# Kernel tuning notes

Measured on AMD Instinct MI355X. Metric: run time of the kernel, lower is better.

## Reference

```python
import jax, jax.numpy as jnp
import numpy as np

# Circuit geometry (matches QNN(sequence_length=16384, quantum_layer_quantity=4, output_quantity=64, entangler='basic'))
SEQ_LEN = 16384
N_ADDR = 14                      # ceil(log2(16384))
N_DATA = 4                       # UNIQUE_NUCLEOTIDE_QUANTITY
N_WIRES = N_ADDR + N_DATA        # 18
DIM = 2 ** N_WIRES               # 262144
N_LAYERS = 4
OUT = 64
BATCH = 32


def _apply_rx(state, theta, w):
    """Apply RX(theta) on wire w (wire 0 = most significant bit)."""
    c = jnp.cos(theta / 2).astype(jnp.complex64)
    s = (-1j * jnp.sin(theta / 2)).astype(jnp.complex64)
    U = jnp.stack([jnp.stack([c, s]), jnp.stack([s, c])])  # [2,2]
    B = state.shape[0]
    st = state.reshape(B, 2 ** w, 2, -1)
    st = jnp.einsum('ij,bajc->baic', U, st)
    return st.reshape(B, DIM)


def _apply_cnot(state, c, t):
    """CNOT with control wire c, target wire t."""
    B = state.shape[0]
    st = state.reshape((B,) + (2,) * N_WIRES)
    c_ax, t_ax = 1 + c, 1 + t
    p0 = jnp.take(st, 0, axis=c_ax)
    p1 = jnp.take(st, 1, axis=c_ax)
    t_ax_r = t_ax - 1 if t_ax > c_ax else t_ax
    p1 = jnp.flip(p1, axis=t_ax_r)  # X on target within control=1 block
    st = jnp.stack([p0, p1], axis=c_ax)
    return st.reshape(B, DIM)


def _circuit_probs(x, qweights):
    # Encoding: address register stays |0...0>, so among all multi-controlled
    # BasisEmbeddings only index 0 (control pattern all zeros) applies its X
    # gates. Resulting basis state index = bits of x[:,0,:] on the 4 data
    # wires (least-significant bits), address bits = 0.
    bits = x[:, 0, :]  # [B, 4]
    pw = jnp.asarray([8, 4, 2, 1], dtype=jnp.int32)
    idx = jnp.sum(bits * pw, axis=-1)  # [B]
    state = jax.nn.one_hot(idx, DIM, dtype=jnp.complex64)  # [B, DIM]
    # BasicEntanglerLayers: per layer, RX on every wire then a CNOT ring.
    for l in range(N_LAYERS):
        for w in range(N_WIRES):
            state = _apply_rx(state, qweights[l, w], w)
        for w in range(N_WIRES):
            state = _apply_cnot(state, w, (w + 1) % N_WIRES)
    return jnp.abs(state) ** 2  # qml.probs over all wires -> [B, DIM] float32


def setup_inputs() -> dict:
    key = jax.random.key(0)
    kx, kw, kW = jax.random.split(key, 3)
    x = jax.random.randint(kx, (BATCH, SEQ_LEN, N_DATA), 0, 2, dtype=jnp.int32)
    qweights = jax.random.uniform(kw, (N_LAYERS, N_WIRES), dtype=jnp.float32,
                                  maxval=2.0 * np.pi)
    W = jax.random.normal(kW, (OUT, DIM), dtype=jnp.float32) / np.sqrt(DIM)
    b = jnp.zeros((OUT,), dtype=jnp.float32)
    return {"x": x, "qweights": qweights, "W": W, "b": b}


def reference(x, qweights, W, b):
    probs = _circuit_probs(x, qweights)          # [B, 2^18]
    logits = probs @ W.T + b                     # [B, 64]
    return jax.nn.sigmoid(logits)
```

## Files before the change

kernel.cpp:

```cpp
#include <hip/hip_runtime.h>
#include <math.h>


#define DIM (1 << 18)
#define NW 18
#define CH 128
#define CPB 4
#define NMM 512
#define PAD16(i) ((i) + ((i) >> 4))

typedef short short8 __attribute__((ext_vector_type(8)));
typedef float f32x4  __attribute__((ext_vector_type(4)));

__device__ __forceinline__ unsigned perm18(unsigned i) {
    unsigned s = i;
    s ^= s >> 1; s ^= s >> 2; s ^= s >> 4; s ^= s >> 8; s ^= s >> 16;
    unsigned out = s & 0x1FFFFu;
    out |= ((s ^ (i >> 17)) & 1u) << 17;
    return out;
}
__device__ __forceinline__ unsigned pinv18(unsigned b) {
    unsigned t = b & 0x1FFFFu;
    unsigned u = (t ^ (t >> 1)) & 0xFFFFu;
    unsigned i17 = ((b >> 17) ^ t) & 1u;
    unsigned i16 = ((t >> 16) ^ i17) & 1u;
    return u | (i16 << 16) | (i17 << 17);
}
__device__ __forceinline__ void bfly(float2& a0, float2& a1, float c, float s) {
    float2 n0 = make_float2(c * a0.x + s * a1.y, c * a0.y - s * a1.x);
    float2 n1 = make_float2(c * a1.x + s * a0.y, c * a1.y - s * a0.x);
    a0 = n0; a1 = n1;
}
__device__ __forceinline__ short f2bf(float x) {
    unsigned u = __float_as_uint(x);
    return (short)((u + 0x7FFFu + ((u >> 16) & 1u)) >> 16);
}

constexpr unsigned cX1M[33] = {
    0x001,0x002,0x004,0x008,0x010,0x020,0x040,0x080,0x100,0x200,0x400,0x800,
    0xC01,0xC03,0xC06,0xC0C,0xC18,0xC30,0xC60,0xCC0,0xD80,0xA00,0xC00,
    0xA01,0x602,0x605,0x60A,0x614,0x628,0x650,0x6A0,0x740,0x600};
constexpr unsigned char cX1A[33] = {
    35,34,33,32,31,30,29,28,27,20,19,18,
    53,52,51,50,49,48,47,46,45,37,36,
    71,70,69,68,67,66,65,64,63,54};
constexpr unsigned cX2M[21] = {
    0x004,0x008,0x010,0x020,0x040,0x080,
    0x606,0x60C,0x618,0x630,0x660,0x6C0,0x780,
    0x305,0x30A,0x314,0x328,0x350,0x3A0,0x240,0x180};
constexpr unsigned char cX2A[21] = {
    26,25,24,23,22,21,
    44,43,42,41,40,39,38,
    62,61,60,59,58,57,56,55};

constexpr int ctzc(unsigned x) { int n = 0; while (!(x & 1u)) { x >>= 1; ++n; } return n; }

template<unsigned M1, unsigned M2, int T, int NT>
__device__ __forceinline__ void pairR(float2* t, float2 g1, float2 g2) {
    constexpr unsigned z1 = M1 & (0u - M1);
    constexpr bool sw = (M2 & z1) != 0u;
    constexpr unsigned M2p = sw ? (M1 ^ M2) : M2;
    constexpr unsigned z2 = M2p & (0u - M2p);
    constexpr unsigned zl = (z1 < z2) ? z1 : z2;
    constexpr unsigned zh = (z1 < z2) ? z2 : z1;
    constexpr int pl = ctzc(zl);
    constexpr int ph = ctzc(zh);
#pragma unroll
    for (int it = 0; it < (T / 4) / NT; ++it) {
        unsigned k = (unsigned)threadIdx.x + (unsigned)(it * NT);
        unsigned i = ((k >> pl) << (pl + 1)) | (k & (zl - 1u));
        i = ((i >> ph) << (ph + 1)) | (i & (zh - 1u));
        int iA = PAD16((int)i), iB = PAD16((int)(i ^ M1));
        int iC = PAD16((int)(i ^ M2p)), iD = PAD16((int)(i ^ M1 ^ M2p));
        float2 A = t[iA], B = t[iB], C = t[iC], D = t[iD];
        bfly(A, B, g1.x, g1.y); bfly(C, D, g1.x, g1.y);
        if (sw) { bfly(A, D, g2.x, g2.y); bfly(B, C, g2.x, g2.y); }
        else    { bfly(A, C, g2.x, g2.y); bfly(B, D, g2.x, g2.y); }
        t[iA] = A; t[iB] = B; t[iC] = C; t[iD] = D;
    }
}
template<unsigned M, int T, int NT>
__device__ __forceinline__ void singleR(float2* t, float2 g) {
    constexpr unsigned z = M & (0u - M);
    constexpr int p = ctzc(z);
#pragma unroll
    for (int it = 0; it < (T / 2) / NT; ++it) {
        unsigned k = (unsigned)threadIdx.x + (unsigned)(it * NT);
        unsigned i = ((k >> p) << (p + 1)) | (k & (z - 1u));
        int i0 = PAD16((int)i), i1 = PAD16((int)(i ^ M));
        float2 A = t[i0], B = t[i1];
        bfly(A, B, g.x, g.y);
        t[i0] = A; t[i1] = B;
    }
}

__global__ __launch_bounds__(1024) void kX1(float2* __restrict__ out, const float* __restrict__ qw) {
    __shared__ float2 t[4352];
    __shared__ float2 g[33];
    int tid = threadIdx.x;
    if (tid < 33) { float th = qw[cX1A[tid]] * 0.5f; g[tid] = make_float2(cosf(th), sinf(th)); }
    float c0[NW], s0[NW];
#pragma unroll
    for (int w = 0; w < NW; ++w) { float th = qw[w] * 0.5f; c0[w] = cosf(th); s0[w] = sinf(th); }
    unsigned blk = blockIdx.x;
#pragma unroll
    for (int r = 0; r < 4; ++r) {
        int l = tid + 1024 * r;
        unsigned b = ((unsigned)l & 511u) | (blk << 9) | (((unsigned)l >> 9) << 15);
        unsigned i = pinv18(b);
        float m = 1.f;
#pragma unroll
        for (int p = 0; p < 18; ++p) m *= ((i >> p) & 1u) ? s0[17 - p] : c0[17 - p];
        int k4 = __popc(i) & 3;
        float2 a;
        if      (k4 == 0) a = make_float2( m, 0.f);
        else if (k4 == 1) a = make_float2(0.f, -m);
        else if (k4 == 2) a = make_float2(-m, 0.f);
        else              a = make_float2(0.f,  m);
        t[PAD16(l)] = a;
    }
    __syncthreads();
#define RX1(a) pairR<cX1M[a], cX1M[(a)+1], 4096, 1024>(t, g[a], g[(a)+1]); __syncthreads();
    RX1(0) RX1(2) RX1(4) RX1(6) RX1(8) RX1(10) RX1(12) RX1(14)
    RX1(16) RX1(18) RX1(20) RX1(22) RX1(24) RX1(26) RX1(28) RX1(30)
#undef RX1
    singleR<cX1M[32], 4096, 1024>(t, g[32]);
    __syncthreads();
#pragma unroll
    for (int r = 0; r < 4; ++r) {
        int l = tid + 1024 * r;
        unsigned b = ((unsigned)l & 511u) | (blk << 9) | (((unsigned)l >> 9) << 15);
        out[b] = t[PAD16(l)];
    }
}

__global__ __launch_bounds__(512) void kX2(const float2* __restrict__ in, float* __restrict__ probs,
                                           const float* __restrict__ qw) {
    __shared__ float2 t[2176];
    __shared__ float2 g[21];
    int tid = threadIdx.x;
    if (tid < 21) { float th = qw[cX2A[tid]] * 0.5f; g[tid] = make_float2(cosf(th), sinf(th)); }
    unsigned blk = blockIdx.x;
#pragma unroll
    for (int r = 0; r < 4; ++r) {
        int l = tid + 512 * r;
        t[PAD16(l)] = in[blk | ((unsigned)l << 7)];
    }
    __syncthreads();
#define RX2(a) pairR<cX2M[a], cX2M[(a)+1], 2048, 512>(t, g[a], g[(a)+1]); __syncthreads();
    RX2(0) RX2(2) RX2(4) RX2(6) RX2(8) RX2(10) RX2(12) RX2(14) RX2(16) RX2(18)
#undef RX2
    singleR<cX2M[20], 2048, 512>(t, g[20]);
    __syncthreads();
#pragma unroll
    for (int r = 0; r < 4; ++r) {
        int l = tid + 512 * r;
        unsigned b = blk | ((unsigned)l << 7);
        unsigned pb = perm18(perm18(perm18(b)));
        float2 a = t[PAD16(l)];
        probs[pb] = a.x * a.x + a.y * a.y;
    }
}

__global__ __launch_bounds__(256) void k_mm(const float* __restrict__ p0,
                                            const float* __restrict__ W,
                                            float* __restrict__ partial) {
    __shared__ short Wl[64][136];
    __shared__ short Pl[16][136];
    __shared__ unsigned Tsh[16];
    int tid = threadIdx.x;
    if (tid < 16) {
        unsigned v = (unsigned)tid;
#pragma unroll
        for (int r = 0; r < 4; ++r) v = perm18(v);
        Tsh[tid] = v;
    }
    __syncthreads();

    unsigned d00 = (unsigned)blockIdx.x * (CH * CPB);
    int wrow = tid >> 5;
    int wcol = (tid & 31) * 4;
    int prow = tid >> 7;
    int pcol = tid & 127;
    unsigned Tp[8];
#pragma unroll
    for (int t = 0; t < 8; ++t) Tp[t] = Tsh[prow + 2 * t];

    int lane = tid & 63, wv = tid >> 6;
    int arow = lane & 15, kg = (lane >> 4) * 8;
    f32x4 acc = {0.f, 0.f, 0.f, 0.f};
    float4 wr[8];
    float  pr[8];

#pragma unroll
    for (int t = 0; t < 8; ++t)
        wr[t] = *(const float4*)&W[(size_t)(wrow + 8 * t) * DIM + d00 + wcol];
#pragma unroll
    for (int t = 0; t < 8; ++t)
        pr[t] = p0[(d00 ^ (Tp[t] & ~127u)) + pcol];
#pragma unroll
    for (int t = 0; t < 8; ++t) {
        short4 b = make_short4(f2bf(wr[t].x), f2bf(wr[t].y), f2bf(wr[t].z), f2bf(wr[t].w));
        *(short4*)&Wl[wrow + 8 * t][wcol] = b;
    }
#pragma unroll
    for (int t = 0; t < 8; ++t)
        Pl[prow + 2 * t][pcol ^ (Tp[t] & 127u)] = f2bf(pr[t]);
    __syncthreads();

    for (int cc = 0; cc < CPB; ++cc) {
        if (cc + 1 < CPB) {
            unsigned d1 = d00 + (unsigned)(cc + 1) * CH;
#pragma unroll
            for (int t = 0; t < 8; ++t)
                wr[t] = *(const float4*)&W[(size_t)(wrow + 8 * t) * DIM + d1 + wcol];
#pragma unroll
            for (int t = 0; t < 8; ++t)
                pr[t] = p0[(d1 ^ (Tp[t] & ~127u)) + pcol];
        }
#pragma unroll
        for (int kk = 0; kk < 4; ++kk) {
            short8 a = *(const short8*)&Pl[arow][kk * 32 + kg];
            short8 b = *(const short8*)&Wl[16 * wv + arow][kk * 32 + kg];
            acc = __builtin_amdgcn_mfma_f32_16x16x32_bf16(a, b, acc, 0, 0, 0);
        }
        __syncthreads();
        if (cc + 1 < CPB) {
#pragma unroll
            for (int t = 0; t < 8; ++t) {
                short4 b = make_short4(f2bf(wr[t].x), f2bf(wr[t].y), f2bf(wr[t].z), f2bf(wr[t].w));
                *(short4*)&Wl[wrow + 8 * t][wcol] = b;
            }
#pragma unroll
            for (int t = 0; t < 8; ++t)
                Pl[prow + 2 * t][pcol ^ (Tp[t] & 127u)] = f2bf(pr[t]);
            __syncthreads();
        }
    }

    float* dst = partial + (size_t)blockIdx.x * 1024;
#pragma unroll
    for (int r = 0; r < 4; ++r) {
        int jrow = (lane >> 4) * 4 + r;
        dst[jrow * 64 + 16 * wv + (lane & 15)] = acc[r];
    }
}

__global__ __launch_bounds__(256) void k_finalize(const float* __restrict__ partial,
                                                  const float* __restrict__ bias,
                                                  const int* __restrict__ x,
                                                  float* __restrict__ out) {
    int b = blockIdx.x;
    int tid = threadIdx.x;
    int ji = tid & 15, ci = tid >> 4;
    int jo = b * 16 + ji;
    float sum = 0.f;
#pragma unroll 8
    for (int c = ci; c < NMM; c += 16)
        sum += partial[(size_t)c * 1024 + jo];
    __shared__ float red[16][17];
    __shared__ float lg[16];
    __shared__ int sidx[32];
    red[ci][ji] = sum;
    if (tid < 32) {
        const int* xb = x + (size_t)tid * (16384 * 4);
        sidx[tid] = 8 * xb[0] + 4 * xb[1] + 2 * xb[2] + xb[3];
    }
    __syncthreads();
    if (ci == 0) {
        float s = 0.f;
#pragma unroll
        for (int k = 0; k < 16; ++k) s += red[k][ji];
        lg[ji] = s + bias[jo & 63];
    }
    __syncthreads();
    int myidx = b >> 2, o0 = (b & 3) * 16;
#pragma unroll
    for (int r = 0; r < 2; ++r) {
        int slot = tid + 256 * r;
        int bb = slot >> 4, k = slot & 15;
        if (sidx[bb] == myidx) {
            float z = lg[k];
            out[bb * 64 + o0 + k] = 1.f / (1.f + expf(-z));
        }
    }
}

extern "C" void kernel_launch(void* const* d_in, const int* in_sizes, int n_in,
                              void* d_out, int out_size, void* d_ws, size_t ws_size,
                              hipStream_t stream) {
    const int*   x    = (const int*)d_in[0];
    const float* qw   = (const float*)d_in[1];
    const float* W    = (const float*)d_in[2];
    const float* bias = (const float*)d_in[3];
    float* out = (float*)d_out;

    char* ws = (char*)d_ws;
    float2*   buf0    = (float2*)(ws + (1ull << 20));
    float*    probs   = (float*)(ws + (8ull << 20));
    float*    partial = (float*)(ws + (16ull << 20));

    kX1<<<64, 1024, 0, stream>>>(buf0, qw);
    kX2<<<128, 512, 0, stream>>>(buf0, probs, qw);
    k_mm<<<NMM, 256, 0, stream>>>(probs, W, partial);
    k_finalize<<<64, 256, 0, stream>>>(partial, bias, x, out);
}
```

Measured before the change: 52.15 us.

## Fuse finalize into matmul kernel via atomic ticket counter

Removes the separate finalize launch. The last 64 matmul blocks to finish, chosen by an atomic ticket counter, wait until every block has written its partial sums, then do the reduction, bias add and sigmoid themselves. The counter is reset inside the first kernel so nothing needs an extra memset launch. This saves one kernel launch and its gap, at the cost of spin-waiting and of assuming all blocks are co-resident or at least make forward progress.

```diff
diff --git a/kernel.cpp b/kernel.cpp
--- a/kernel.cpp
+++ b/kernel.cpp
@@ -94,10 +94,13 @@
     }
 }
 
-__global__ __launch_bounds__(1024) void kX1(float2* __restrict__ out, const float* __restrict__ qw) {
+__global__ __launch_bounds__(1024) void kX1(float2* __restrict__ out, const float* __restrict__ qw,
+                                            unsigned* __restrict__ ctr) {
     __shared__ float2 t[4352];
     __shared__ float2 g[33];
     int tid = threadIdx.x;
+    if (blockIdx.x == 0 && tid == 0)
+        __hip_atomic_store(ctr, 0u, __ATOMIC_RELAXED, __HIP_MEMORY_SCOPE_AGENT);
     if (tid < 33) { float th = qw[cX1A[tid]] * 0.5f; g[tid] = make_float2(cosf(th), sinf(th)); }
     float c0[NW], s0[NW];
 #pragma unroll
@@ -164,10 +167,18 @@
 
 __global__ __launch_bounds__(256) void k_mm(const float* __restrict__ p0,
                                             const float* __restrict__ W,
-                                            float* __restrict__ partial) {
+                                            float* __restrict__ partial,
+                                            const int* __restrict__ x,
+                                            const float* __restrict__ bias,
+                                            float* __restrict__ out,
+                                            unsigned* __restrict__ ctr) {
     __shared__ short Wl[64][136];
     __shared__ short Pl[16][136];
     __shared__ unsigned Tsh[16];
+    __shared__ unsigned tik;
+    __shared__ float red[16][17];
+    __shared__ float lg[16];
+    __shared__ int sidx[32];
     int tid = threadIdx.x;
     if (tid < 16) {
         unsigned v = (unsigned)tid;
@@ -242,25 +253,31 @@
 #pragma unroll
     for (int r = 0; r < 4; ++r) {
         int jrow = (lane >> 4) * 4 + r;
-        dst[jrow * 64 + 16 * wv + (lane & 15)] = acc[r];
-    }
-}
-
-__global__ __launch_bounds__(256) void k_finalize(const float* __restrict__ partial,
-                                                  const float* __restrict__ bias,
-                                                  const int* __restrict__ x,
-                                                  float* __restrict__ out) {
-    int b = blockIdx.x;
-    int tid = threadIdx.x;
+        __hip_atomic_store(&dst[jrow * 64 + 16 * wv + (lane & 15)], acc[r],
+                           __ATOMIC_RELAXED, __HIP_MEMORY_SCOPE_AGENT);
+    }
+    __syncthreads();
+
+    if (tid == 0)
+        tik = __hip_atomic_fetch_add(ctr, 1u, __ATOMIC_RELEASE, __HIP_MEMORY_SCOPE_AGENT);
+    __syncthreads();
+    unsigned ticket = tik;
+    if (ticket < (unsigned)(NMM - 64)) return;
+    int b = (int)(ticket - (NMM - 64));
+
+    if (tid == 0) {
+        while (__hip_atomic_load(ctr, __ATOMIC_RELAXED, __HIP_MEMORY_SCOPE_AGENT) < (unsigned)NMM)
+            __builtin_amdgcn_s_sleep(4);
+    }
+    __syncthreads();
+
     int ji = tid & 15, ci = tid >> 4;
     int jo = b * 16 + ji;
     float sum = 0.f;
 #pragma unroll 8
     for (int c = ci; c < NMM; c += 16)
-        sum += partial[(size_t)c * 1024 + jo];
-    __shared__ float red[16][17];
-    __shared__ float lg[16];
-    __shared__ int sidx[32];
+        sum += __hip_atomic_load(&partial[(size_t)c * 1024 + jo],
+                                 __ATOMIC_RELAXED, __HIP_MEMORY_SCOPE_AGENT);
     red[ci][ji] = sum;
     if (tid < 32) {
         const int* xb = x + (size_t)tid * (16384 * 4);
@@ -296,12 +313,12 @@
     float* out = (float*)d_out;
 
     char* ws = (char*)d_ws;
+    unsigned* ctr     = (unsigned*)ws;
     float2*   buf0    = (float2*)(ws + (1ull << 20));
     float*    probs   = (float*)(ws + (8ull << 20));
     float*    partial = (float*)(ws + (16ull << 20));
 
-    kX1<<<64, 1024, 0, stream>>>(buf0, qw);
+    kX1<<<64, 1024, 0, stream>>>(buf0, qw, ctr);
     kX2<<<128, 512, 0, stream>>>(buf0, probs, qw);
-    k_mm<<<NMM, 256, 0, stream>>>(probs, W, partial);
-    k_finalize<<<64, 256, 0, stream>>>(partial, bias, x, out);
-}
+    k_mm<<<NMM, 256, 0, stream>>>(probs, W, partial, x, bias, out, ctr);
+}
```

After: 58.72 us. 12.6% more time.

## Apply rotation gates three at a time in registers to cut LDS passes

Applied to the files above, without the earlier changes.

Replaces the pairwise and single-gate LDS butterfly passes with a triR routine that loads eight amplitudes per thread, applies three rotation gates in registers, and stores them back. This cuts the number of shared-memory round trips and __syncthreads barriers per kernel. kX1 also applies its first three gates in registers before the first LDS store. Block sizes are halved (1024→512, 512→256) so each thread handles eight elements. The trade-off is more registers per thread and fewer threads, which may expose LDS latency and lower occupancy.

```diff
diff --git a/kernel.cpp b/kernel.cpp
--- a/kernel.cpp
+++ b/kernel.cpp
@@ -55,46 +55,56 @@
 
 constexpr int ctzc(unsigned x) { int n = 0; while (!(x & 1u)) { x >>= 1; ++n; } return n; }
 
-template<unsigned M1, unsigned M2, int T, int NT>
-__device__ __forceinline__ void pairR(float2* t, float2 g1, float2 g2) {
+template<int C>
+__device__ __forceinline__ void applyG(float2* E, float2 g) {
+    constexpr int L = C & (-C);
+#pragma unroll
+    for (int v = 0; v < 8; ++v)
+        if (!(v & L)) bfly(E[v], E[v ^ C], g.x, g.y);
+}
+
+template<unsigned M1, unsigned M2, unsigned M3, int T, int NT>
+__device__ __forceinline__ void triR(float2* t, float2 g1, float2 g2, float2 g3) {
     constexpr unsigned z1 = M1 & (0u - M1);
-    constexpr bool sw = (M2 & z1) != 0u;
-    constexpr unsigned M2p = sw ? (M1 ^ M2) : M2;
-    constexpr unsigned z2 = M2p & (0u - M2p);
-    constexpr unsigned zl = (z1 < z2) ? z1 : z2;
-    constexpr unsigned zh = (z1 < z2) ? z2 : z1;
-    constexpr int pl = ctzc(zl);
-    constexpr int ph = ctzc(zh);
-#pragma unroll
-    for (int it = 0; it < (T / 4) / NT; ++it) {
+    constexpr unsigned B2a = (M2 & z1) ? (M2 ^ M1) : M2;
+    constexpr unsigned z2 = B2a & (0u - B2a);
+    constexpr unsigned B1a = (M1 & z2) ? (M1 ^ B2a) : M1;
+    constexpr unsigned B3a = (M3 & z1) ? (M3 ^ B1a) : M3;
+    constexpr unsigned B3b = (B3a & z2) ? (B3a ^ B2a) : B3a;
+    constexpr unsigned z3 = B3b & (0u - B3b);
+    constexpr unsigned B1 = (B1a & z3) ? (B1a ^ B3b) : B1a;
+    constexpr unsigned B2 = (B2a & z3) ? (B2a ^ B3b) : B2a;
+    constexpr unsigned B3 = B3b;
+    constexpr int c1 = ((M1 & z1) ? 1 : 0) | ((M1 & z2) ? 2 : 0) | ((M1 & z3) ? 4 : 0);
+    constexpr int c2 = ((M2 & z1) ? 1 : 0) | ((M2 & z2) ? 2 : 0) | ((M2 & z3) ? 4 : 0);
+    constexpr int c3 = ((M3 & z1) ? 1 : 0) | ((M3 & z2) ? 2 : 0) | ((M3 & z3) ? 4 : 0);
+    constexpr int q1 = ctzc(z1), q2 = ctzc(z2), q3 = ctzc(z3);
+    constexpr int pa = (q1 < q2 ? (q1 < q3 ? q1 : q3) : (q2 < q3 ? q2 : q3));
+    constexpr int pc = (q1 > q2 ? (q1 > q3 ? q1 : q3) : (q2 > q3 ? q2 : q3));
+    constexpr int pb = q1 + q2 + q3 - pa - pc;
+#pragma unroll
+    for (int it = 0; it < (T / 8) / NT; ++it) {
         unsigned k = (unsigned)threadIdx.x + (unsigned)(it * NT);
-        unsigned i = ((k >> pl) << (pl + 1)) | (k & (zl - 1u));
-        i = ((i >> ph) << (ph + 1)) | (i & (zh - 1u));
-        int iA = PAD16((int)i), iB = PAD16((int)(i ^ M1));
-        int iC = PAD16((int)(i ^ M2p)), iD = PAD16((int)(i ^ M1 ^ M2p));
-        float2 A = t[iA], B = t[iB], C = t[iC], D = t[iD];
-        bfly(A, B, g1.x, g1.y); bfly(C, D, g1.x, g1.y);
-        if (sw) { bfly(A, D, g2.x, g2.y); bfly(B, C, g2.x, g2.y); }
-        else    { bfly(A, C, g2.x, g2.y); bfly(B, D, g2.x, g2.y); }
-        t[iA] = A; t[iB] = B; t[iC] = C; t[iD] = D;
-    }
-}
-template<unsigned M, int T, int NT>
-__device__ __forceinline__ void singleR(float2* t, float2 g) {
-    constexpr unsigned z = M & (0u - M);
-    constexpr int p = ctzc(z);
-#pragma unroll
-    for (int it = 0; it < (T / 2) / NT; ++it) {
-        unsigned k = (unsigned)threadIdx.x + (unsigned)(it * NT);
-        unsigned i = ((k >> p) << (p + 1)) | (k & (z - 1u));
-        int i0 = PAD16((int)i), i1 = PAD16((int)(i ^ M));
-        float2 A = t[i0], B = t[i1];
-        bfly(A, B, g.x, g.y);
-        t[i0] = A; t[i1] = B;
-    }
-}
-
-__global__ __launch_bounds__(1024) void kX1(float2* __restrict__ out, const float* __restrict__ qw) {
+        unsigned i = ((k >> pa) << (pa + 1)) | (k & ((1u << pa) - 1u));
+        i = ((i >> pb) << (pb + 1)) | (i & ((1u << pb) - 1u));
+        i = ((i >> pc) << (pc + 1)) | (i & ((1u << pc) - 1u));
+        int idx[8];
+        float2 E[8];
+#pragma unroll
+        for (int v = 0; v < 8; ++v) {
+            unsigned e = i ^ ((v & 1) ? B1 : 0u) ^ ((v & 2) ? B2 : 0u) ^ ((v & 4) ? B3 : 0u);
+            idx[v] = PAD16((int)e);
+            E[v] = t[idx[v]];
+        }
+        applyG<c1>(E, g1);
+        applyG<c2>(E, g2);
+        applyG<c3>(E, g3);
+#pragma unroll
+        for (int v = 0; v < 8; ++v) t[idx[v]] = E[v];
+    }
+}
+
+__global__ __launch_bounds__(512) void kX1(float2* __restrict__ out, const float* __restrict__ qw) {
     __shared__ float2 t[4352];
     __shared__ float2 g[33];
     int tid = threadIdx.x;
@@ -103,38 +113,40 @@
 #pragma unroll
     for (int w = 0; w < NW; ++w) { float th = qw[w] * 0.5f; c0[w] = cosf(th); s0[w] = sinf(th); }
     unsigned blk = blockIdx.x;
-#pragma unroll
-    for (int r = 0; r < 4; ++r) {
-        int l = tid + 1024 * r;
+    float2 E[8];
+#pragma unroll
+    for (int v = 0; v < 8; ++v) {
+        int l = 8 * tid + v;
         unsigned b = ((unsigned)l & 511u) | (blk << 9) | (((unsigned)l >> 9) << 15);
         unsigned i = pinv18(b);
         float m = 1.f;
 #pragma unroll
         for (int p = 0; p < 18; ++p) m *= ((i >> p) & 1u) ? s0[17 - p] : c0[17 - p];
         int k4 = __popc(i) & 3;
-        float2 a;
-        if      (k4 == 0) a = make_float2( m, 0.f);
-        else if (k4 == 1) a = make_float2(0.f, -m);
-        else if (k4 == 2) a = make_float2(-m, 0.f);
-        else              a = make_float2(0.f,  m);
-        t[PAD16(l)] = a;
-    }
-    __syncthreads();
-#define RX1(a) pairR<cX1M[a], cX1M[(a)+1], 4096, 1024>(t, g[a], g[(a)+1]); __syncthreads();
-    RX1(0) RX1(2) RX1(4) RX1(6) RX1(8) RX1(10) RX1(12) RX1(14)
-    RX1(16) RX1(18) RX1(20) RX1(22) RX1(24) RX1(26) RX1(28) RX1(30)
-#undef RX1
-    singleR<cX1M[32], 4096, 1024>(t, g[32]);
-    __syncthreads();
-#pragma unroll
-    for (int r = 0; r < 4; ++r) {
-        int l = tid + 1024 * r;
+        if      (k4 == 0) E[v] = make_float2( m, 0.f);
+        else if (k4 == 1) E[v] = make_float2(0.f, -m);
+        else if (k4 == 2) E[v] = make_float2(-m, 0.f);
+        else              E[v] = make_float2(0.f,  m);
+    }
+    __syncthreads();
+    applyG<1>(E, g[0]);
+    applyG<2>(E, g[1]);
+    applyG<4>(E, g[2]);
+#pragma unroll
+    for (int v = 0; v < 8; ++v) t[PAD16(8 * tid + v)] = E[v];
+    __syncthreads();
+#define TX1(a) triR<cX1M[a], cX1M[(a)+1], cX1M[(a)+2], 4096, 512>(t, g[a], g[(a)+1], g[(a)+2]); __syncthreads();
+    TX1(3) TX1(6) TX1(9) TX1(12) TX1(15) TX1(18) TX1(21) TX1(24) TX1(27) TX1(30)
+#undef TX1
+#pragma unroll
+    for (int r = 0; r < 8; ++r) {
+        int l = tid + 512 * r;
         unsigned b = ((unsigned)l & 511u) | (blk << 9) | (((unsigned)l >> 9) << 15);
         out[b] = t[PAD16(l)];
     }
 }
 
-__global__ __launch_bounds__(512) void kX2(const float2* __restrict__ in, float* __restrict__ probs,
+__global__ __launch_bounds__(256) void kX2(const float2* __restrict__ in, float* __restrict__ probs,
                                            const float* __restrict__ qw) {
     __shared__ float2 t[2176];
     __shared__ float2 g[21];
@@ -142,19 +154,17 @@
     if (tid < 21) { float th = qw[cX2A[tid]] * 0.5f; g[tid] = make_float2(cosf(th), sinf(th)); }
     unsigned blk = blockIdx.x;
 #pragma unroll
-    for (int r = 0; r < 4; ++r) {
-        int l = tid + 512 * r;
+    for (int r = 0; r < 8; ++r) {
+        int l = tid + 256 * r;
         t[PAD16(l)] = in[blk | ((unsigned)l << 7)];
     }
     __syncthreads();
-#define RX2(a) pairR<cX2M[a], cX2M[(a)+1], 2048, 512>(t, g[a], g[(a)+1]); __syncthreads();
-    RX2(0) RX2(2) RX2(4) RX2(6) RX2(8) RX2(10) RX2(12) RX2(14) RX2(16) RX2(18)
-#undef RX2
-    singleR<cX2M[20], 2048, 512>(t, g[20]);
-    __syncthreads();
-#pragma unroll
-    for (int r = 0; r < 4; ++r) {
-        int l = tid + 512 * r;
+#define TX2(a) triR<cX2M[a], cX2M[(a)+1], cX2M[(a)+2], 2048, 256>(t, g[a], g[(a)+1], g[(a)+2]); __syncthreads();
+    TX2(0) TX2(3) TX2(6) TX2(9) TX2(12) TX2(15) TX2(18)
+#undef TX2
+#pragma unroll
+    for (int r = 0; r < 8; ++r) {
+        int l = tid + 256 * r;
         unsigned b = blk | ((unsigned)l << 7);
         unsigned pb = perm18(perm18(perm18(b)));
         float2 a = t[PAD16(l)];
@@ -300,8 +310,8 @@
     float*    probs   = (float*)(ws + (8ull << 20));
     float*    partial = (float*)(ws + (16ull << 20));
 
-    kX1<<<64, 1024, 0, stream>>>(buf0, qw);
-    kX2<<<128, 512, 0, stream>>>(buf0, probs, qw);
+    kX1<<<64, 512, 0, stream>>>(buf0, qw);
+    kX2<<<128, 256, 0, stream>>>(buf0, probs, qw);
     k_mm<<<NMM, 256, 0, stream>>>(probs, W, partial);
     k_finalize<<<64, 256, 0, stream>>>(partial, bias, x, out);
 }
```

After: 49.44 us. 1.05x faster.
